# Kernel optimization log

Measured on AMD Instinct MI355X. Metric: run time of the kernel, lower is better.

The kernel has to match this reference:

```python
import jax, jax.numpy as jnp
import numpy as np

G = 512          # number of graphs
N = 512          # nodes per graph (equal-sized graphs)
NN = G * N       # total nodes
EG = 8192        # edges per graph (avg degree 16)
C_IN, HID, OUT, K = 128, 32, 2, 20
LATENT = HID * 2 + 1  # 65 = conv1 kernel size & stride


def _gcn(x, W, b, src, dst, deg_inv_sqrt):
    """GCNConv with self-loops: out = D^-1/2 (A+I) D^-1/2 (x W) + b."""
    h = x @ W                                        # [NN, out]
    norm = deg_inv_sqrt[src] * deg_inv_sqrt[dst]     # [E]
    agg = jnp.zeros_like(h).at[dst].add(h[src] * norm[:, None])
    # self-loop message: norm_ii = deg_inv_sqrt[i]^2
    agg = agg + h * (deg_inv_sqrt * deg_inv_sqrt)[:, None]
    return agg + b


def setup_inputs() -> dict:
    key = jax.random.key(0)
    ks = jax.random.split(key, 24)
    x = jax.random.normal(ks[0], (NN, C_IN), jnp.float32)
    offs = (jnp.arange(G, dtype=jnp.int32) * N)[:, None]
    src = (jax.random.randint(ks[1], (G, EG), 0, N, jnp.int32) + offs).reshape(-1)
    dst = (jax.random.randint(ks[2], (G, EG), 0, N, jnp.int32) + offs).reshape(-1)
    edge_index = jnp.stack([src, dst])               # [2, G*EG]
    batch = jnp.repeat(jnp.arange(G, dtype=jnp.int32), N)

    def lin(k, fan_in, shape):
        return jax.random.normal(k, shape, jnp.float32) / np.sqrt(fan_in)

    return {
        "x": x, "edge_index": edge_index, "batch": batch,
        "W0": lin(ks[3], C_IN, (C_IN, HID)), "b0": jnp.zeros((HID,), jnp.float32),
        "W1": lin(ks[4], HID, (HID, HID)),   "b1": jnp.zeros((HID,), jnp.float32),
        "W2": lin(ks[5], HID, (HID, 1)),     "b2": jnp.zeros((1,), jnp.float32),
        "conv1_w": lin(ks[6], LATENT, (16, 1, LATENT)), "conv1_b": jnp.zeros((16,), jnp.float32),
        "conv2_w": lin(ks[7], 16 * 5, (32, 16, 5)),     "conv2_b": jnp.zeros((32,), jnp.float32),
        "lin1_w": lin(ks[8], 192, (192, 128)), "lin1_b": jnp.zeros((128,), jnp.float32),
        "lin2_w": lin(ks[9], 128, (128, OUT)), "lin2_b": jnp.zeros((OUT,), jnp.float32),
    }


def reference(x, edge_index, batch, W0, b0, W1, b1, W2, b2,
              conv1_w, conv1_b, conv2_w, conv2_b,
              lin1_w, lin1_b, lin2_w, lin2_b):
    src, dst = edge_index[0], edge_index[1]
    deg = jnp.zeros((NN,), jnp.float32).at[dst].add(1.0) + 1.0  # +1 self-loop
    dis = jax.lax.rsqrt(deg)

    x1 = jnp.tanh(_gcn(x,  W0, b0, src, dst, dis))   # [NN, 32]
    x2 = jnp.tanh(_gcn(x1, W1, b1, src, dst, dis))   # [NN, 32]
    x3 = jnp.tanh(_gcn(x2, W2, b2, src, dst, dis))   # [NN, 1]
    feat = jnp.concatenate([x1, x2, x3], axis=-1)    # [NN, 65]

    # global_sort_pool: equal-sized contiguous graphs -> reshape, sort by last
    # channel (descending) within each graph, take top-k nodes.
    fg = feat.reshape(G, N, LATENT)
    idx = jnp.argsort(-fg[..., -1], axis=1)[:, :K]                 # [G, K]
    pooled = jnp.take_along_axis(fg, idx[:, :, None], axis=1)      # [G, K, 65]

    # conv1: Conv1d(1,16,kernel=65,stride=65) over flattened [G,1,K*65]
    # == per-sorted-node matmul with the 65-wide kernel.
    h = jax.nn.relu(jnp.einsum('gkc,oc->gok', pooled, conv1_w[:, 0, :])
                    + conv1_b[None, :, None])                      # [G, 16, K]
    h = h.reshape(G, 16, K // 2, 2).max(-1)                        # MaxPool1d(2,2) -> [G,16,10]
    h = jax.nn.relu(
        jax.lax.conv_general_dilated(h, conv2_w, (1,), 'VALID',
                                     dimension_numbers=('NCH', 'OIH', 'NCH'))
        + conv2_b[None, :, None])                                  # [G, 32, 6]
    h = h.reshape(G, -1)                                           # [G, 192]
    h = jax.nn.relu(h @ lin1_w + lin1_b)
    # dropout is identity in eval mode
    return h @ lin2_w + lin2_b                                     # [G, 2]
```

## Files before the change

### kernel.cpp

```cpp
#include <hip/hip_runtime.h>
#include <math.h>

#define G_ 512
#define N_ 512
#define NN_ (G_*N_)
#define EG_ 8192
#define CIN_ 128
#define HID_ 32
#define K_ 20
#define LAT_ 65
#define NSTRIPE 4
#define SW 8
#define HP 514

#define EPS_REL 1.8e-7f

__global__ __launch_bounds__(512) void csr2_kernel(const int* __restrict__ src,
                                                   const int* __restrict__ dst,
                                                   unsigned short* __restrict__ srcl,
                                                   int* __restrict__ gstart,
                                                   double* __restrict__ disd) {
    __shared__ int cnt[N_];
    __shared__ int startv[N_];
    __shared__ int tmpv[N_];
    __shared__ int cursor[N_];
    __shared__ unsigned short binE[EG_];
    int g = blockIdx.x, tid = threadIdx.x;
    const int* ds = dst + (size_t)g * EG_;
    const int* ss = src + (size_t)g * EG_;
    int nb = g * N_;

    cnt[tid] = 0;
    __syncthreads();
    for (int e = tid; e < EG_; e += 512) atomicAdd(&cnt[ds[e] - nb], 1);
    __syncthreads();

    startv[tid] = cnt[tid];
    __syncthreads();
    for (int off = 1; off < N_; off <<= 1) {
        tmpv[tid] = startv[tid] + (tid >= off ? startv[tid - off] : 0);
        __syncthreads();
        startv[tid] = tmpv[tid];
        __syncthreads();
    }

    int excl = startv[tid] - cnt[tid];
    cursor[tid] = excl;
    gstart[g * (N_ + 1) + tid] = excl;
    if (tid == 0) gstart[g * (N_ + 1) + N_] = EG_;
    disd[nb + tid] = 1.0 / sqrt((double)(cnt[tid] + 1));
    __syncthreads();

    for (int e = tid; e < EG_; e += 512) {
        int d = ds[e] - nb;
        int slot = atomicAdd(&cursor[d], 1);
        binE[slot] = (unsigned short)e;
    }
    __syncthreads();

    {
        int n = cnt[tid];
        for (int i = 1; i < n; ++i) {
            unsigned short key = binE[excl + i];
            int j = i - 1;
            while (j >= 0 && binE[excl + j] > key) {
                binE[excl + j + 1] = binE[excl + j];
                --j;
            }
            binE[excl + j + 1] = key;
        }
    }
    __syncthreads();

    for (int i = tid; i < EG_; i += 512) {
        int e = binE[i];
        srcl[(size_t)g * EG_ + i] = (unsigned short)(ss[e] - nb);
    }
}

template <int CI>
__global__ __launch_bounds__(256) void mm_kernel(const float* __restrict__ xin,
                                                 const float* __restrict__ W,
                                                 double* __restrict__ h) {
    __shared__ float sx[64][CI + 4];
    __shared__ float sW[CI][HID_];
    int tid = threadIdx.x;
    for (int i = tid; i < CI * HID_; i += 256) sW[i / HID_][i % HID_] = W[i];
    size_t base = (size_t)blockIdx.x * 64;
    const float4* xsrc = (const float4*)(xin + base * CI);
    for (int i = tid; i < 64 * CI / 4; i += 256) {
        int row = i / (CI / 4), col = (i % (CI / 4)) * 4;
        *(float4*)&sx[row][col] = xsrc[i];
    }
    __syncthreads();

    int o2 = tid & 15, q = tid >> 4;
    int n0 = q * 4;
    double acc[4][2];
#pragma unroll
    for (int j = 0; j < 4; ++j) { acc[j][0] = 0.0; acc[j][1] = 0.0; }

    for (int c = 0; c < CI; c += 4) {
        double w0a = (double)sW[c][o2],     w0b = (double)sW[c][o2 + 16];
        double w1a = (double)sW[c + 1][o2], w1b = (double)sW[c + 1][o2 + 16];
        double w2a = (double)sW[c + 2][o2], w2b = (double)sW[c + 2][o2 + 16];
        double w3a = (double)sW[c + 3][o2], w3b = (double)sW[c + 3][o2 + 16];
#pragma unroll
        for (int j = 0; j < 4; ++j) {
            float4 v = *(const float4*)&sx[n0 + j][c];
            double vx = (double)v.x, vy = (double)v.y,
                   vz = (double)v.z, vw = (double)v.w;
            acc[j][0] = fma(vx, w0a, acc[j][0]);
            acc[j][0] = fma(vy, w1a, acc[j][0]);
            acc[j][0] = fma(vz, w2a, acc[j][0]);
            acc[j][0] = fma(vw, w3a, acc[j][0]);
            acc[j][1] = fma(vx, w0b, acc[j][1]);
            acc[j][1] = fma(vy, w1b, acc[j][1]);
            acc[j][1] = fma(vz, w2b, acc[j][1]);
            acc[j][1] = fma(vw, w3b, acc[j][1]);
        }
    }
#pragma unroll
    for (int j = 0; j < 4; ++j) {
#pragma unroll
        for (int p = 0; p < 2; ++p) {
            int o = o2 + 16 * p;
            h[(((size_t)(o >> 3)) * NN_ + base + n0 + j) * SW + (o & 7)] = acc[j][p];
        }
    }
}

__global__ __launch_bounds__(512) void agg_kernel(const double* __restrict__ h,
                                                  const unsigned short* __restrict__ srcl,
                                                  const int* __restrict__ gstart,
                                                  const double* __restrict__ disd,
                                                  const float* __restrict__ bias,
                                                  float* __restrict__ xoutf) {
    __shared__ double hd2[SW * HP];
    __shared__ unsigned short ssrc[EG_];
    __shared__ unsigned short sstart[N_ + 2];
    __shared__ double sdis[N_];
    int g = blockIdx.x, st = blockIdx.y, tid = threadIdx.x;
    size_t nbase = (size_t)g * N_;

    for (int i = tid; i < EG_; i += 512) ssrc[i] = srcl[(size_t)g * EG_ + i];
    for (int i = tid; i <= N_; i += 512) sstart[i] = (unsigned short)gstart[g * (N_ + 1) + i];
    sdis[tid] = disd[nbase + tid];
    __syncthreads();

    const double* hraw = h + ((size_t)st * NN_ + nbase) * SW;
    for (int i = tid; i < N_ * SW; i += 512) {
        int s = i >> 3, oc = i & 7;
        hd2[oc * HP + s] = hraw[i] * sdis[s];
    }
    __syncthreads();

    int oc = tid & 7, grp = tid >> 3;
    const double* hrow = hd2 + oc * HP;
    double b = (double)bias[st * SW + oc];

    int e0[8], e1[8];
    double a[8];
    int mx = 0;
#pragma unroll
    for (int j = 0; j < 8; ++j) {
        int n = grp + j * 64;
        e0[j] = sstart[n];
        e1[j] = sstart[n + 1];
        a[j] = 0.0;
        int d = e1[j] - e0[j];
        mx = d > mx ? d : mx;
    }
    for (int t = 0; t < mx; ++t) {
#pragma unroll
        for (int j = 0; j < 8; ++j) {
            int idx = e0[j] + t;
            if (idx < e1[j]) {
                int s = ssrc[idx];
                a[j] += hrow[s];
            }
        }
    }
#pragma unroll
    for (int j = 0; j < 8; ++j) {
        int n = grp + j * 64;
        double dn = sdis[n];
        double v = a[j] * dn + hrow[n] * dn + b;
        xoutf[(nbase + n) * HID_ + st * SW + oc] = tanhf((float)v);
    }
}

__global__ __launch_bounds__(512) void gcn3_kernel(const float* __restrict__ xin,
                                                   const float* __restrict__ W2,
                                                   const float* __restrict__ b2,
                                                   const unsigned short* __restrict__ srcl,
                                                   const int* __restrict__ gstart,
                                                   const double* __restrict__ disd,
                                                   float* __restrict__ x3f) {
    __shared__ double h1[N_];
    __shared__ unsigned short ssrc[EG_];
    __shared__ int sstart[N_ + 1];
    __shared__ double sdis[N_];
    int g = blockIdx.x, tid = threadIdx.x;
    size_t nbase = (size_t)g * N_;

    for (int i = tid; i < EG_; i += 512) ssrc[i] = srcl[(size_t)g * EG_ + i];
    for (int i = tid; i <= N_; i += 512) sstart[i] = gstart[g * (N_ + 1) + i];
    int n = tid;
    {
        double a = 0.0;
#pragma unroll
        for (int c = 0; c < HID_; ++c)
            a = fma((double)xin[(nbase + n) * HID_ + c], (double)W2[c], a);
        h1[n] = a;
        sdis[n] = disd[nbase + n];
    }
    __syncthreads();

    int e0 = sstart[n], e1 = sstart[n + 1];
    double a = 0.0;
    for (int e = e0; e < e1; ++e) {
        int s = ssrc[e];
        a += h1[s] * sdis[s];
    }
    double dn = sdis[n];
    double v = a * dn + h1[n] * dn * dn + (double)b2[0];
    x3f[nbase + n] = (float)tanh(v);
}

__global__ __launch_bounds__(256) void head_kernel(const float* __restrict__ x1,
                                                   const float* __restrict__ x2,
                                                   const float* __restrict__ x3f,
                                                   const float* __restrict__ c1w,
                                                   const float* __restrict__ c1b,
                                                   const float* __restrict__ c2w,
                                                   const float* __restrict__ c2b,
                                                   const float* __restrict__ l1w,
                                                   const float* __restrict__ l1b,
                                                   const float* __restrict__ l2w,
                                                   const float* __restrict__ l2b,
                                                   float* __restrict__ out) {
    int g = blockIdx.x;
    size_t nbase = (size_t)g * N_;
    __shared__ float sv[N_];
    __shared__ int   topk[K_];
    __shared__ float pooled[K_][LAT_];
    __shared__ float c1[16][K_];
    __shared__ float mp[16][10];
    __shared__ float c2[32 * 6];
    __shared__ float l1[128];

    for (int i = threadIdx.x; i < K_; i += 256) topk[i] = i;
    for (int i = threadIdx.x; i < N_; i += 256) sv[i] = x3f[nbase + i];
    __syncthreads();

    for (int i = threadIdx.x; i < N_; i += 256) {
        float v = sv[i];
        int rank = 0;
        for (int j = 0; j < N_; ++j) {
            float u = sv[j];
            float mag = fmaxf(fabsf(u), fabsf(v));
            bool tie = fabsf(u - v) <= EPS_REL * mag;
            bool beats = tie ? (j < i) : (u > v);
            rank += beats;
        }
        if (rank < K_) topk[rank] = i;
    }
    __syncthreads();

    for (int i = threadIdx.x; i < K_ * LAT_; i += 256) {
        int k = i / LAT_, c = i % LAT_;
        int node = topk[k];
        float f;
        if (c < HID_)            f = x1[(nbase + node) * HID_ + c];
        else if (c < 2 * HID_)   f = x2[(nbase + node) * HID_ + (c - HID_)];
        else                     f = sv[node];
        pooled[k][c] = f;
    }
    __syncthreads();

    for (int i = threadIdx.x; i < 16 * K_; i += 256) {
        int o = i / K_, k = i % K_;
        float acc = c1b[o];
        for (int c = 0; c < LAT_; ++c) acc += pooled[k][c] * c1w[o * LAT_ + c];
        c1[o][k] = fmaxf(acc, 0.f);
    }
    __syncthreads();

    for (int i = threadIdx.x; i < 160; i += 256) {
        int o = i / 10, t = i % 10;
        mp[o][t] = fmaxf(c1[o][2 * t], c1[o][2 * t + 1]);
    }
    __syncthreads();

    for (int i = threadIdx.x; i < 192; i += 256) {
        int o = i / 6, t = i % 6;
        float acc = c2b[o];
        for (int ic = 0; ic < 16; ++ic)
#pragma unroll
            for (int j = 0; j < 5; ++j)
                acc += mp[ic][t + j] * c2w[(o * 16 + ic) * 5 + j];
        c2[o * 6 + t] = fmaxf(acc, 0.f);
    }
    __syncthreads();

    for (int i = threadIdx.x; i < 128; i += 256) {
        float acc = l1b[i];
        for (int c = 0; c < 192; ++c) acc += c2[c] * l1w[c * 128 + i];
        l1[i] = fmaxf(acc, 0.f);
    }
    __syncthreads();

    for (int i = threadIdx.x; i < 2; i += 256) {
        float acc = l2b[i];
        for (int c = 0; c < 128; ++c) acc += l1[c] * l2w[c * 2 + i];
        out[g * 2 + i] = acc;
    }
}

extern "C" void kernel_launch(void* const* d_in, const int* in_sizes, int n_in,
                              void* d_out, int out_size, void* d_ws, size_t ws_size,
                              hipStream_t stream) {
    const float* x   = (const float*)d_in[0];
    const int*   ei  = (const int*)d_in[1];
    const float* W0  = (const float*)d_in[3];
    const float* b0  = (const float*)d_in[4];
    const float* W1  = (const float*)d_in[5];
    const float* b1  = (const float*)d_in[6];
    const float* W2  = (const float*)d_in[7];
    const float* b2  = (const float*)d_in[8];
    const float* c1w = (const float*)d_in[9];
    const float* c1b = (const float*)d_in[10];
    const float* c2w = (const float*)d_in[11];
    const float* c2b = (const float*)d_in[12];
    const float* l1w = (const float*)d_in[13];
    const float* l1b = (const float*)d_in[14];
    const float* l2w = (const float*)d_in[15];
    const float* l2b = (const float*)d_in[16];

    const int* src = ei;
    const int* dst = ei + (size_t)G_ * EG_;

    char* wsb = (char*)d_ws;
    double* h64  = (double*)wsb;                 wsb += (size_t)NN_ * HID_ * 8;
    unsigned short* srcl = (unsigned short*)wsb; wsb += (size_t)G_ * EG_ * 2;
    int* gstart = (int*)wsb;                     wsb += (size_t)G_ * (N_ + 1) * 4;
    double* disd = (double*)wsb;                 wsb += (size_t)NN_ * 8;
    float*  x3f  = (float*)wsb;                  wsb += (size_t)NN_ * 4;
    float*  x1f  = (float*)wsb;                  wsb += (size_t)NN_ * HID_ * 4;
    float*  x2f  = (float*)wsb;                  wsb += (size_t)NN_ * HID_ * 4;

    dim3 agrid(G_, NSTRIPE);
    csr2_kernel<<<G_, 512, 0, stream>>>(src, dst, srcl, gstart, disd);
    mm_kernel<CIN_><<<NN_ / 64, 256, 0, stream>>>(x, W0, h64);
    agg_kernel<<<agrid, 512, 0, stream>>>(h64, srcl, gstart, disd, b0, x1f);
    mm_kernel<HID_><<<NN_ / 64, 256, 0, stream>>>(x1f, W1, h64);
    agg_kernel<<<agrid, 512, 0, stream>>>(h64, srcl, gstart, disd, b1, x2f);
    gcn3_kernel<<<G_, 512, 0, stream>>>(x2f, W2, b2, srcl, gstart, disd, x3f);
    head_kernel<<<G_, 256, 0, stream>>>(x1f, x2f, x3f, c1w, c1b, c2w, c2b,
                                        l1w, l1b, l2w, l2b, (float*)d_out);
}
```

Before: 390.3 us.

## Sort nodes by degree to balance per-thread edge loops in aggregation

The CSR build kernel now computes, per graph, a permutation of nodes ordered by in-degree using an O(N) rank count per thread. The aggregation kernel assigns each thread 8 consecutive degree-sorted nodes instead of strided nodes, so the max-degree loop bound per thread sits close to its actual work and divergent idle iterations shrink. It also changes the LDS row padding from 514 to 513 doubles and reads degree scaling directly from global memory instead of shared memory. The extra rank loop adds about 512 shared reads per thread to the CSR kernel, and output stores become scattered.

```diff
diff --git a/kernel.cpp b/kernel.cpp
--- a/kernel.cpp
+++ b/kernel.cpp
@@ -11,7 +11,7 @@
 #define LAT_ 65
 #define NSTRIPE 4
 #define SW 8
-#define HP 514
+#define HP 513
 
 #define EPS_REL 1.8e-7f
 
@@ -19,6 +19,7 @@
                                                    const int* __restrict__ dst,
                                                    unsigned short* __restrict__ srcl,
                                                    int* __restrict__ gstart,
+                                                   unsigned short* __restrict__ nperm,
                                                    double* __restrict__ disd) {
     __shared__ int cnt[N_];
     __shared__ int startv[N_];
@@ -34,6 +35,16 @@
     __syncthreads();
     for (int e = tid; e < EG_; e += 512) atomicAdd(&cnt[ds[e] - nb], 1);
     __syncthreads();
+
+    {
+        int mydeg = cnt[tid];
+        int rank = 0;
+        for (int j = 0; j < N_; ++j) {
+            int dj = cnt[j];
+            rank += (dj < mydeg) || (dj == mydeg && j < tid);
+        }
+        nperm[g * N_ + rank] = (unsigned short)tid;
+    }
 
     startv[tid] = cnt[tid];
     __syncthreads();
@@ -133,25 +144,27 @@
 __global__ __launch_bounds__(512) void agg_kernel(const double* __restrict__ h,
                                                   const unsigned short* __restrict__ srcl,
                                                   const int* __restrict__ gstart,
+                                                  const unsigned short* __restrict__ nperm,
                                                   const double* __restrict__ disd,
                                                   const float* __restrict__ bias,
                                                   float* __restrict__ xoutf) {
     __shared__ double hd2[SW * HP];
     __shared__ unsigned short ssrc[EG_];
     __shared__ unsigned short sstart[N_ + 2];
-    __shared__ double sdis[N_];
+    __shared__ unsigned short sperm[N_];
     int g = blockIdx.x, st = blockIdx.y, tid = threadIdx.x;
     size_t nbase = (size_t)g * N_;
 
     for (int i = tid; i < EG_; i += 512) ssrc[i] = srcl[(size_t)g * EG_ + i];
     for (int i = tid; i <= N_; i += 512) sstart[i] = (unsigned short)gstart[g * (N_ + 1) + i];
-    sdis[tid] = disd[nbase + tid];
+    sperm[tid] = nperm[g * N_ + tid];
     __syncthreads();
 
     const double* hraw = h + ((size_t)st * NN_ + nbase) * SW;
+    const double* dg = disd + nbase;
     for (int i = tid; i < N_ * SW; i += 512) {
         int s = i >> 3, oc = i & 7;
-        hd2[oc * HP + s] = hraw[i] * sdis[s];
+        hd2[oc * HP + s] = hraw[i] * dg[s];
     }
     __syncthreads();
 
@@ -159,12 +172,13 @@
     const double* hrow = hd2 + oc * HP;
     double b = (double)bias[st * SW + oc];
 
-    int e0[8], e1[8];
+    int nn[8], e0[8], e1[8];
     double a[8];
     int mx = 0;
 #pragma unroll
     for (int j = 0; j < 8; ++j) {
-        int n = grp + j * 64;
+        int n = sperm[grp * 8 + j];
+        nn[j] = n;
         e0[j] = sstart[n];
         e1[j] = sstart[n + 1];
         a[j] = 0.0;
@@ -183,8 +197,8 @@
     }
 #pragma unroll
     for (int j = 0; j < 8; ++j) {
-        int n = grp + j * 64;
-        double dn = sdis[n];
+        int n = nn[j];
+        double dn = dg[n];
         double v = a[j] * dn + hrow[n] * dn + b;
         xoutf[(nbase + n) * HID_ + st * SW + oc] = tanhf((float)v);
     }
@@ -345,17 +359,18 @@
     double* h64  = (double*)wsb;                 wsb += (size_t)NN_ * HID_ * 8;
     unsigned short* srcl = (unsigned short*)wsb; wsb += (size_t)G_ * EG_ * 2;
     int* gstart = (int*)wsb;                     wsb += (size_t)G_ * (N_ + 1) * 4;
+    unsigned short* nperm = (unsigned short*)wsb; wsb += (size_t)G_ * N_ * 2;
     double* disd = (double*)wsb;                 wsb += (size_t)NN_ * 8;
     float*  x3f  = (float*)wsb;                  wsb += (size_t)NN_ * 4;
     float*  x1f  = (float*)wsb;                  wsb += (size_t)NN_ * HID_ * 4;
     float*  x2f  = (float*)wsb;                  wsb += (size_t)NN_ * HID_ * 4;
 
     dim3 agrid(G_, NSTRIPE);
-    csr2_kernel<<<G_, 512, 0, stream>>>(src, dst, srcl, gstart, disd);
+    csr2_kernel<<<G_, 512, 0, stream>>>(src, dst, srcl, gstart, nperm, disd);
     mm_kernel<CIN_><<<NN_ / 64, 256, 0, stream>>>(x, W0, h64);
-    agg_kernel<<<agrid, 512, 0, stream>>>(h64, srcl, gstart, disd, b0, x1f);
+    agg_kernel<<<agrid, 512, 0, stream>>>(h64, srcl, gstart, nperm, disd, b0, x1f);
     mm_kernel<HID_><<<NN_ / 64, 256, 0, stream>>>(x1f, W1, h64);
-    agg_kernel<<<agrid, 512, 0, stream>>>(h64, srcl, gstart, disd, b1, x2f);
+    agg_kernel<<<agrid, 512, 0, stream>>>(h64, srcl, gstart, nperm, disd, b1, x2f);
     gcn3_kernel<<<G_, 512, 0, stream>>>(x2f, W2, b2, srcl, gstart, disd, x3f);
     head_kernel<<<G_, 256, 0, stream>>>(x1f, x2f, x3f, c1w, c1b, c2w, c2b,
                                         l1w, l1b, l2w, l2b, (float*)d_out);
```

Measured after the change: 384.9 us. About the same (-1.4%).
